# Kernel optimization log

Measured on AMD Instinct MI355X. Metric: run time of the kernel, lower is better.

## Reference

```python
import jax, jax.numpy as jnp
import numpy as np

N, E, IN, H, C, B, DD = 50000, 800000, 128, 4, 32, 64, 32
HC = H * C  # 128 = hidden_dim * num_heads


def setup_inputs() -> dict:
    key = jax.random.key(0)
    ks = jax.random.split(key, 28)
    r = lambda i, shape: jax.random.normal(ks[i], shape, jnp.float32) * 0.05
    return {
        "x": jax.random.normal(ks[0], (N, IN), jnp.float32),
        "domain": jax.random.normal(ks[1], (B, DD), jnp.float32),
        "Wl1": r(2, (HC, IN)), "bl1": r(3, (HC,)),
        "Wr1": r(4, (HC, IN)), "br1": r(5, (HC,)),
        "att1": r(6, (H, C)), "bias1": r(7, (HC,)),
        "Wl2": r(8, (HC, HC)), "bl2": r(9, (HC,)),
        "Wr2": r(10, (HC, HC)), "br2": r(11, (HC,)),
        "att2": r(12, (H, C)), "bias2": r(13, (HC,)),
        "Wres": r(14, (HC, IN)), "bres": r(15, (HC,)),
        "Wd": r(16, (64, DD)), "bd": r(17, (64,)),
        "Wg": r(18, (HC, HC)), "bg": r(19, (HC,)),
        "Wf1": r(20, (128, HC + 64)), "bf1": r(21, (128,)),
        "Wf2": r(22, (64, 128)), "bf2": r(23, (64,)),
        "Wf3": r(24, (1, 64)), "bf3": r(25, (1,)),
        "edge_index": jax.random.randint(ks[26], (2, E), 0, N),
        "batch": jnp.sort(jax.random.randint(ks[27], (N,), 0, B)),
    }


def gatv2_conv(x, src, dst, Wl, bl, Wr, br, att, bias):
    """PyG GATv2Conv, add_self_loops=False, concat heads, eval (no dropout)."""
    n = x.shape[0]
    xl = (x @ Wl.T + bl).reshape(n, H, C)  # source-side transform (lin_l)
    xr = (x @ Wr.T + br).reshape(n, H, C)  # target-side transform (lin_r)
    e = jax.nn.leaky_relu(xl[src] + xr[dst], 0.2)            # [E,H,C]
    s = jnp.einsum('ehc,hc->eh', e, att)                      # [E,H]
    smax = jax.ops.segment_max(s, dst, num_segments=n)        # per-dst max
    a = jnp.exp(s - smax[dst])
    denom = jax.ops.segment_sum(a, dst, num_segments=n)
    alpha = a / denom[dst]                                    # segment softmax
    out = jax.ops.segment_sum(alpha[:, :, None] * xl[src], dst, num_segments=n)
    return out.reshape(n, HC) + bias


def reference(x, domain, Wl1, bl1, Wr1, br1, att1, bias1,
              Wl2, bl2, Wr2, br2, att2, bias2,
              Wres, bres, Wd, bd, Wg, bg,
              Wf1, bf1, Wf2, bf2, Wf3, bf3,
              edge_index, batch):
    src, dst = edge_index[0], edge_index[1]
    res = x @ Wres.T + bres
    h = jax.nn.relu(gatv2_conv(x, src, dst, Wl1, bl1, Wr1, br1, att1, bias1)) + res
    h = jax.nn.relu(gatv2_conv(h, src, dst, Wl2, bl2, Wr2, br2, att2, bias2)) + h
    # global mean pool over graphs
    sums = jax.ops.segment_sum(h, batch, num_segments=B)
    counts = jax.ops.segment_sum(jnp.ones((h.shape[0],), h.dtype), batch, num_segments=B)
    pooled = sums / jnp.maximum(counts, 1.0)[:, None]
    g = jax.nn.relu(pooled @ Wg.T + bg)
    d = jax.nn.relu(domain @ Wd.T + bd)
    z = jnp.concatenate([g, d], axis=1)
    z = jax.nn.relu(z @ Wf1.T + bf1)
    z = jax.nn.relu(z @ Wf2.T + bf2)
    return (z @ Wf3.T + bf3).squeeze()
```

## Files before the change

### kernel.cpp

```cpp
#include <hip/hip_runtime.h>
#include <math.h>

#define NN 50000
#define NE 800000
#define FD 128
#define NB 64
#define NBUK 196
#define CHK 3125
#define NSC 1024
#define CHK2 782
#define CAP 6144
#define NBLK 782

typedef __attribute__((ext_vector_type(8))) short short8v;
typedef __attribute__((ext_vector_type(4))) float f32x4;
typedef _Float16 h2 __attribute__((ext_vector_type(2)));
typedef _Float16 h8 __attribute__((ext_vector_type(8)));

__device__ __forceinline__ unsigned short f2h(float f) {
  return __builtin_bit_cast(unsigned short, (_Float16)f);
}
__device__ __forceinline__ float h2f(unsigned short u) {
  return (float)__builtin_bit_cast(_Float16, u);
}

__device__ __forceinline__ size_t img_base(int n, int lane) {
  int lrow = n & 63, blk = n >> 6;
  int kh = lane >> 4, s7 = (lane >> 1) & 7, off4 = (lane & 1) * 4;
  return (size_t)blk * 8192 + kh * 4096 + lrow * 64 + 8 * (s7 ^ (lrow & 7)) + off4;
}

__global__ __launch_bounds__(256) void k_prep1(const float* __restrict__ W0,
    const float* __restrict__ W1, const float* __restrict__ W2,
    const float* __restrict__ W3, const float* __restrict__ W4,
    unsigned short* __restrict__ wh, unsigned short* __restrict__ wl,
    const int* __restrict__ dst, int* __restrict__ bcnt,
    const float* __restrict__ x, unsigned short* __restrict__ ximg) {
  __shared__ int bh[NBUK];
  int bx = blockIdx.x;
  if (bx < 256) {
    int t = threadIdx.x;
    for (int i = t; i < NBUK; i += 256) bh[i] = 0;
    __syncthreads();
    int e0 = bx * CHK, e1 = e0 + CHK;
    if (e1 > NE) e1 = NE;
    for (int e = e0 + t; e < e1; e += 256) atomicAdd(&bh[dst[e] >> 8], 1);
    __syncthreads();
    for (int i = t; i < NBUK; i += 256) if (bh[i]) atomicAdd(&bcnt[i], bh[i]);
  } else if (bx < 296) {
    int id = (bx - 256) * 256 + threadIdx.x;
    if (id >= 5 * 2048) return;
    int w = id >> 11, rem = id & 2047;
    int row = rem >> 4, slot = rem & 15;
    const float* Wp = (w == 0) ? W0 : (w == 1) ? W1 : (w == 2) ? W2 : (w == 3) ? W3 : W4;
    const float* sp = &Wp[row * 128 + slot * 8];
    int kh = slot >> 3, s7 = slot & 7;
    int d = ((w * 2 + kh) * 8192) + row * 64 + 8 * (s7 ^ (row & 7));
    short8v hi, lo;
    #pragma unroll
    for (int j = 0; j < 8; ++j) {
      float f = sp[j];
      _Float16 hv = (_Float16)f;
      _Float16 lv = (_Float16)(f - (float)hv);
      hi[j] = (short)__builtin_bit_cast(unsigned short, hv);
      lo[j] = (short)__builtin_bit_cast(unsigned short, lv);
    }
    *(short8v*)&wh[d] = hi;
    *(short8v*)&wl[d] = lo;
  } else {
    int id = (bx - 296) * 256 + threadIdx.x;
    int row = id >> 4, slot = id & 15;
    const float* sp = &x[(size_t)row * 128 + slot * 8];
    int blk = row >> 6, lrow = row & 63, kh = slot >> 3, s7 = slot & 7;
    size_t hoff = (size_t)blk * 8192 + kh * 4096 + lrow * 64 + 8 * (s7 ^ (lrow & 7));
    short8v hv;
    #pragma unroll
    for (int j = 0; j < 8; ++j)
      hv[j] = (short)f2h(sp[j]);
    *(short8v*)&ximg[hoff] = hv;
  }
}

__global__ __launch_bounds__(256) void k_bscan(const int* __restrict__ bcnt,
                                               int* __restrict__ bbase,
                                               int* __restrict__ bcur) {
  __shared__ int wsum[4];
  int t = threadIdx.x;
  int v = (t < NBUK) ? bcnt[t] : 0;
  int lane = t & 63, wv = t >> 6;
  int s = v;
  #pragma unroll
  for (int off = 1; off < 64; off <<= 1) {
    int y = __shfl_up(s, off, 64);
    if (lane >= off) s += y;
  }
  if (lane == 63) wsum[wv] = s;
  __syncthreads();
  if (t == 0) {
    int r = 0;
    #pragma unroll
    for (int i = 0; i < 4; ++i) { int x = wsum[i]; wsum[i] = r; r += x; }
  }
  __syncthreads();
  int excl = s - v + wsum[wv];
  if (t < NBUK) { bbase[t] = excl; bcur[t] = excl; }
  if (t == NBUK - 1) bbase[NBUK] = excl + v;
}

__global__ __launch_bounds__(256) void k_bscatter(const int* __restrict__ src,
    const int* __restrict__ dst, int* __restrict__ bcur, int* __restrict__ tmpv) {
  __shared__ int bh[NBUK];
  __shared__ int bb[NBUK];
  __shared__ int brun[NBUK];
  int t = threadIdx.x;
  int e0 = blockIdx.x * CHK2, e1 = e0 + CHK2;
  if (e1 > NE) e1 = NE;
  for (int i = t; i < NBUK; i += 256) { bh[i] = 0; brun[i] = 0; }
  __syncthreads();
  for (int e = e0 + t; e < e1; e += 256) atomicAdd(&bh[dst[e] >> 8], 1);
  __syncthreads();
  for (int i = t; i < NBUK; i += 256)
    bb[i] = bh[i] ? atomicAdd(&bcur[i], bh[i]) : 0;
  __syncthreads();
  for (int e = e0 + t; e < e1; e += 256) {
    int d = dst[e];
    int bk = d >> 8;
    int p = bb[bk] + atomicAdd(&brun[bk], 1);
    tmpv[p] = (src[e] << 8) | (d & 255);
  }
}

__device__ __forceinline__ void linm2_body(
    const unsigned short* __restrict__ aimg,
    const unsigned short* __restrict__ wh_img, const unsigned short* __restrict__ wl_img,
    int wimg, const float* __restrict__ bias,
    _Float16* __restrict__ out_h, int blk, char* smem) {
  unsigned short* s_a  = (unsigned short*)smem;
  unsigned short* s_wh = s_a + 4096;
  unsigned short* s_wl = s_wh + 8192;
  const int tid = threadIdx.x;
  const int lane = tid & 63;
  const int wv = tid >> 6;
  const int m0 = (wv >> 2) * 32;
  const int n0 = (wv & 3) * 32;
  const int rbase = blk * 64;
  const int g = lane >> 4, lr = lane & 15;

  f32x4 acc[2][2];
  #pragma unroll
  for (int mt = 0; mt < 2; ++mt)
    #pragma unroll
    for (int nt = 0; nt < 2; ++nt)
      acc[mt][nt] = (f32x4){0.f, 0.f, 0.f, 0.f};

  for (int kh = 0; kh < 2; ++kh) {
    if (kh) __syncthreads();
    {
      const short8v* asrc = (const short8v*)(aimg + (size_t)blk * 8192 + kh * 4096);
      ((short8v*)s_a)[tid] = asrc[tid];
    }
    {
      const short8v* whs = (const short8v*)(wh_img + (size_t)(wimg * 2 + kh) * 8192);
      const short8v* wls = (const short8v*)(wl_img + (size_t)(wimg * 2 + kh) * 8192);
      short8v* whd = (short8v*)s_wh;
      short8v* wld = (short8v*)s_wl;
      whd[tid] = whs[tid]; whd[512 + tid] = whs[512 + tid];
      wld[tid] = wls[tid]; wld[512 + tid] = wls[512 + tid];
    }
    __syncthreads();
    #pragma unroll
    for (int ks = 0; ks < 2; ++ks) {
      const int slot = ks * 4 + g;
      h8 a[2];
      #pragma unroll
      for (int mt = 0; mt < 2; ++mt) {
        int row = m0 + mt * 16 + lr;
        int idx = row * 64 + 8 * (slot ^ (row & 7));
        a[mt] = __builtin_bit_cast(h8, *(const short8v*)&s_a[idx]);
      }
      #pragma unroll
      for (int nt = 0; nt < 2; ++nt) {
        int row2 = n0 + nt * 16 + lr;
        int idx2 = row2 * 64 + 8 * (slot ^ (row2 & 7));
        h8 bh = __builtin_bit_cast(h8, *(const short8v*)&s_wh[idx2]);
        h8 bl = __builtin_bit_cast(h8, *(const short8v*)&s_wl[idx2]);
        #pragma unroll
        for (int mt = 0; mt < 2; ++mt) {
          acc[mt][nt] = __builtin_amdgcn_mfma_f32_16x16x32_f16(a[mt], bh, acc[mt][nt], 0, 0, 0);
          acc[mt][nt] = __builtin_amdgcn_mfma_f32_16x16x32_f16(a[mt], bl, acc[mt][nt], 0, 0, 0);
        }
      }
    }
  }
  #pragma unroll
  for (int nt = 0; nt < 2; ++nt) {
    float bv = bias[n0 + nt * 16 + lr];
    #pragma unroll
    for (int mt = 0; mt < 2; ++mt)
      #pragma unroll
      for (int i = 0; i < 4; ++i) {
        int r = rbase + m0 + mt * 16 + 4 * g + i;
        if (r < NN) {
          float vv = acc[mt][nt][i] + bv;
          out_h[(size_t)r * 128 + n0 + nt * 16 + lr] = (_Float16)vv;
        }
      }
  }
}

__global__ __launch_bounds__(512, 8) void k_csrlin(
    const int* __restrict__ tmpv, const int* __restrict__ bbase,
    int* __restrict__ offs, int* __restrict__ ssrc,
    const unsigned short* __restrict__ ximg,
    const unsigned short* __restrict__ wh_img, const unsigned short* __restrict__ wl_img,
    const float* __restrict__ bl1, const float* __restrict__ br1, const float* __restrict__ bres,
    _Float16* __restrict__ xl, _Float16* __restrict__ xr,
    _Float16* __restrict__ res) {
  __shared__ __align__(16) char smem[40960];
  int bx = blockIdx.x;
  if (bx < NBUK) {
    int* sdeg = (int*)smem;
    int* scur = sdeg + 256;
    int* wsum = scur + 256;
    int* lsrc = wsum + 16;
    int b = bx, t = threadIdx.x;
    int es = bbase[b], ee = bbase[b + 1];
    int cnt = ee - es;
    if (t < 256) sdeg[t] = 0;
    __syncthreads();
    for (int i = t; i < cnt; i += 512) atomicAdd(&sdeg[tmpv[es + i] & 255], 1);
    __syncthreads();
    int v = 0, s = 0;
    int lane = t & 63, wv = t >> 6;
    if (t < 256) {
      v = sdeg[t];
      s = v;
      #pragma unroll
      for (int off = 1; off < 64; off <<= 1) {
        int y = __shfl_up(s, off, 64);
        if (lane >= off) s += y;
      }
      if (lane == 63) wsum[wv] = s;
    }
    __syncthreads();
    if (t == 0) {
      int r = 0;
      #pragma unroll
      for (int i = 0; i < 4; ++i) { int x2 = wsum[i]; wsum[i] = r; r += x2; }
    }
    __syncthreads();
    if (t < 256) {
      int excl = s - v + wsum[wv];
      scur[t] = excl;
      int node = b * 256 + t;
      if (node < NN) offs[node] = es + excl;
    }
    if (b == 0 && t == 0) offs[NN] = NE;
    __syncthreads();
    if (cnt <= CAP) {
      for (int i = t; i < cnt; i += 512) {
        int pkt = tmpv[es + i];
        int p = atomicAdd(&scur[pkt & 255], 1);
        lsrc[p] = pkt >> 8;
      }
      __syncthreads();
      for (int i = t; i < cnt; i += 512) ssrc[es + i] = lsrc[i];
    } else {
      for (int i = t; i < cnt; i += 512) {
        int pkt = tmpv[es + i];
        int p = atomicAdd(&scur[pkt & 255], 1);
        ssrc[es + p] = pkt >> 8;
      }
    }
  } else {
    int bf = bx - NBUK;
    int w = bf / NBLK, blk = bf % NBLK;
    const float* bias = (w == 0) ? bl1 : (w == 1) ? br1 : bres;
    _Float16* oh = (w == 0) ? xl : (w == 1) ? xr : res;
    linm2_body(ximg, wh_img, wl_img, w, bias, oh, blk, smem);
  }
}

__global__ __launch_bounds__(512, 8) void k_lin2(
    const unsigned short* __restrict__ himg,
    const unsigned short* __restrict__ wh_img, const unsigned short* __restrict__ wl_img,
    const float* __restrict__ bl2, const float* __restrict__ br2,
    _Float16* __restrict__ xl, _Float16* __restrict__ xr) {
  __shared__ __align__(16) char smem[40960];
  int w = blockIdx.y;
  linm2_body(himg, wh_img, wl_img, 3 + w, (w == 0) ? bl2 : br2,
             (w == 0) ? xl : xr, blockIdx.x, smem);
}

__device__ __forceinline__ float4 gat_core(const _Float16* __restrict__ xl,
    const _Float16* __restrict__ xr, const int* __restrict__ offs,
    const int* __restrict__ ssrc, const float* __restrict__ att,
    const float* __restrict__ bias, int n, int lane) {
  float4 att4 = ((const float4*)att)[lane];
  h2 att01 = {(_Float16)att4.x, (_Float16)att4.y};
  h2 att23 = {(_Float16)att4.z, (_Float16)att4.w};
  uint2 xru = ((const uint2*)xr)[(size_t)n * 32 + lane];
  h2 xr01 = __builtin_bit_cast(h2, xru.x);
  h2 xr23 = __builtin_bit_cast(h2, xru.y);
  const h2 k02 = {(_Float16)0.2f, (_Float16)0.2f};
  int e0 = offs[n], e1 = offs[n + 1];
  float den = 0.f;
  float4 acc = make_float4(0.f, 0.f, 0.f, 0.f);
  int e = e0;
  for (; e + 3 < e1; e += 4) {
    uint2 u[4];
    #pragma unroll
    for (int j = 0; j < 4; ++j) {
      int s = ssrc[e + j];
      u[j] = ((const uint2*)xl)[(size_t)s * 32 + lane];
    }
    #pragma unroll
    for (int j = 0; j < 4; ++j) {
      h2 v01 = __builtin_bit_cast(h2, u[j].x);
      h2 v23 = __builtin_bit_cast(h2, u[j].y);
      h2 t01 = v01 + xr01;
      h2 t23 = v23 + xr23;
      h2 l01 = __builtin_elementwise_max(t01, t01 * k02);
      h2 l23 = __builtin_elementwise_max(t23, t23 * k02);
      float p = __builtin_amdgcn_fdot2(l01, att01, 0.f, false);
      p = __builtin_amdgcn_fdot2(l23, att23, p, false);
      p += __shfl_xor(p, 1, 64); p += __shfl_xor(p, 2, 64); p += __shfl_xor(p, 4, 64);
      float w = __expf(p);
      den += w;
      acc.x += w * (float)v01[0];
      acc.y += w * (float)v01[1];
      acc.z += w * (float)v23[0];
      acc.w += w * (float)v23[1];
    }
  }
  for (; e < e1; ++e) {
    int s = ssrc[e];
    uint2 uu = ((const uint2*)xl)[(size_t)s * 32 + lane];
    h2 v01 = __builtin_bit_cast(h2, uu.x);
    h2 v23 = __builtin_bit_cast(h2, uu.y);
    h2 t01 = v01 + xr01;
    h2 t23 = v23 + xr23;
    h2 l01 = __builtin_elementwise_max(t01, t01 * k02);
    h2 l23 = __builtin_elementwise_max(t23, t23 * k02);
    float p = __builtin_amdgcn_fdot2(l01, att01, 0.f, false);
    p = __builtin_amdgcn_fdot2(l23, att23, p, false);
    p += __shfl_xor(p, 1, 64); p += __shfl_xor(p, 2, 64); p += __shfl_xor(p, 4, 64);
    float w = __expf(p);
    den += w;
    acc.x += w * (float)v01[0];
    acc.y += w * (float)v01[1];
    acc.z += w * (float)v23[0];
    acc.w += w * (float)v23[1];
  }
  float inv = (den > 0.f) ? 1.f / den : 0.f;
  float4 b4 = ((const float4*)bias)[lane];
  float4 o;
  o.x = fmaxf(acc.x * inv + b4.x, 0.f);
  o.y = fmaxf(acc.y * inv + b4.y, 0.f);
  o.z = fmaxf(acc.z * inv + b4.z, 0.f);
  o.w = fmaxf(acc.w * inv + b4.w, 0.f);
  return o;
}

__global__ __launch_bounds__(256) void k_gat1(const _Float16* __restrict__ xl,
    const _Float16* __restrict__ xr, const int* __restrict__ offs,
    const int* __restrict__ ssrc, const float* __restrict__ att,
    const float* __restrict__ bias, const _Float16* __restrict__ resid,
    unsigned short* __restrict__ himg) {
  int grp = threadIdx.x >> 5;
  int lane = threadIdx.x & 31;
  int n = blockIdx.x * 8 + grp;
  float4 o = gat_core(xl, xr, offs, ssrc, att, bias, n, lane);
  uint2 ru = ((const uint2*)resid)[(size_t)n * 32 + lane];
  h2 r01 = __builtin_bit_cast(h2, ru.x);
  h2 r23 = __builtin_bit_cast(h2, ru.y);
  o.x += (float)r01[0]; o.y += (float)r01[1];
  o.z += (float)r23[0]; o.w += (float)r23[1];
  size_t base = img_base(n, lane);
  ushort4 hv;
  hv.x = f2h(o.x); hv.y = f2h(o.y); hv.z = f2h(o.z); hv.w = f2h(o.w);
  *(ushort4*)&himg[base] = hv;
}

__global__ __launch_bounds__(256) void k_gatpool(const _Float16* __restrict__ xl,
    const _Float16* __restrict__ xr, const int* __restrict__ offs,
    const int* __restrict__ ssrc, const float* __restrict__ att,
    const float* __restrict__ bias, const unsigned short* __restrict__ himg,
    const int* __restrict__ batch, float* __restrict__ pooled) {
  __shared__ float sm[8][128];
  __shared__ int sbat[8];
  int grp = threadIdx.x >> 5;
  int lane = threadIdx.x & 31;
  int n = blockIdx.x * 8 + grp;
  float4 o = gat_core(xl, xr, offs, ssrc, att, bias, n, lane);
  size_t base = img_base(n, lane);
  ushort4 rh = *(const ushort4*)&himg[base];
  o.x += h2f(rh.x); o.y += h2f(rh.y); o.z += h2f(rh.z); o.w += h2f(rh.w);
  *(float4*)&sm[grp][lane * 4] = o;
  if (threadIdx.x < 8) sbat[threadIdx.x] = batch[blockIdx.x * 8 + threadIdx.x];
  __syncthreads();
  int t = threadIdx.x;
  if (t < 128) {
    float run = sm[0][t];
    int cb = sbat[0];
    #pragma unroll
    for (int g2 = 1; g2 < 8; ++g2) {
      int bb = sbat[g2];
      if (bb != cb) { atomicAdd(&pooled[cb * FD + t], run); run = 0.f; cb = bb; }
      run += sm[g2][t];
    }
    atomicAdd(&pooled[cb * FD + t], run);
  }
}

__global__ __launch_bounds__(128) void k_mlp(const float* __restrict__ pooled,
    const int* __restrict__ batch, const float* __restrict__ domain,
    const float* __restrict__ Wg, const float* __restrict__ bg,
    const float* __restrict__ Wd, const float* __restrict__ bd,
    const float* __restrict__ Wf1, const float* __restrict__ bf1,
    const float* __restrict__ Wf2, const float* __restrict__ bf2,
    const float* __restrict__ Wf3, const float* __restrict__ bf3,
    float* __restrict__ out) {
  __shared__ float z[192];
  __shared__ float z1[128];
  __shared__ float z2[64];
  __shared__ float pm[128];
  __shared__ int cnt;
  int b = blockIdx.x, t = threadIdx.x;
  if (t == 0) {
    int lo = 0, hi = NN;
    while (lo < hi) { int mid = (lo + hi) >> 1; if (batch[mid] < b) lo = mid + 1; else hi = mid; }
    int lb = lo; lo = 0; hi = NN;
    while (lo < hi) { int mid = (lo + hi) >> 1; if (batch[mid] < b + 1) lo = mid + 1; else hi = mid; }
    cnt = lo - lb;
  }
  __syncthreads();
  float invc = 1.f / fmaxf((float)cnt, 1.f);
  pm[t] = pooled[b * FD + t] * invc;
  __syncthreads();
  {
    float a = bg[t];
    for (int k = 0; k < 128; ++k) a += pm[k] * Wg[t * 128 + k];
    z[t] = fmaxf(a, 0.f);
  }
  if (t < 64) {
    float a = bd[t];
    for (int k = 0; k < 32; ++k) a += domain[b * 32 + k] * Wd[t * 32 + k];
    z[128 + t] = fmaxf(a, 0.f);
  }
  __syncthreads();
  {
    float a = bf1[t];
    for (int k = 0; k < 192; ++k) a += z[k] * Wf1[t * 192 + k];
    z1[t] = fmaxf(a, 0.f);
  }
  __syncthreads();
  if (t < 64) {
    float a = bf2[t];
    for (int k = 0; k < 128; ++k) a += z1[k] * Wf2[t * 128 + k];
    z2[t] = fmaxf(a, 0.f);
  }
  __syncthreads();
  if (t < 64) {
    float v = z2[t] * Wf3[t];
    for (int off = 1; off < 64; off <<= 1) v += __shfl_xor(v, off, 64);
    if (t == 0) out[b] = v + bf3[0];
  }
}

extern "C" void kernel_launch(void* const* d_in, const int* in_sizes, int n_in,
                              void* d_out, int out_size, void* d_ws, size_t ws_size,
                              hipStream_t stream) {
  const float* x      = (const float*)d_in[0];
  const float* domain = (const float*)d_in[1];
  const float* Wl1 = (const float*)d_in[2];  const float* bl1 = (const float*)d_in[3];
  const float* Wr1 = (const float*)d_in[4];  const float* br1 = (const float*)d_in[5];
  const float* att1= (const float*)d_in[6];  const float* bias1=(const float*)d_in[7];
  const float* Wl2 = (const float*)d_in[8];  const float* bl2 = (const float*)d_in[9];
  const float* Wr2 = (const float*)d_in[10]; const float* br2 = (const float*)d_in[11];
  const float* att2= (const float*)d_in[12]; const float* bias2=(const float*)d_in[13];
  const float* Wres= (const float*)d_in[14]; const float* bres= (const float*)d_in[15];
  const float* Wd  = (const float*)d_in[16]; const float* bd  = (const float*)d_in[17];
  const float* Wg  = (const float*)d_in[18]; const float* bg  = (const float*)d_in[19];
  const float* Wf1 = (const float*)d_in[20]; const float* bf1 = (const float*)d_in[21];
  const float* Wf2 = (const float*)d_in[22]; const float* bf2 = (const float*)d_in[23];
  const float* Wf3 = (const float*)d_in[24]; const float* bf3 = (const float*)d_in[25];
  const int* ei    = (const int*)d_in[26];
  const int* batch = (const int*)d_in[27];
  const int* esrc = ei;
  const int* edst = ei + NE;
  float* outp = (float*)d_out;

  char* p = (char*)d_ws;
  auto carve = [&](size_t bytes) { char* r = p; p += (bytes + 255) & ~(size_t)255; return r; };
  int* bcnt     = (int*)carve((size_t)NBUK * 4);
  int* bbase    = (int*)carve((size_t)(NBUK + 1) * 4);
  int* bcur     = (int*)carve((size_t)NBUK * 4);
  int* tmpv     = (int*)carve((size_t)NE * 4);
  int* ssrc     = (int*)carve((size_t)NE * 4);
  int* offs     = (int*)carve((size_t)(NN + 1) * 4);
  unsigned short* wh = (unsigned short*)carve((size_t)5 * 2 * 8192 * 2);
  unsigned short* wl = (unsigned short*)carve((size_t)5 * 2 * 8192 * 2);
  unsigned short* ximg = (unsigned short*)carve((size_t)NBLK * 8192 * 2);
  _Float16* xl  = (_Float16*)carve((size_t)NN * FD * 2);
  _Float16* xr  = (_Float16*)carve((size_t)NN * FD * 2);
  _Float16* res = (_Float16*)carve((size_t)NN * FD * 2);
  float* pooled = (float*)carve((size_t)NB * FD * 4);
  unsigned short* himg = ximg;

  hipMemsetAsync(bcnt, 0, (size_t)NBUK * 4, stream);
  hipMemsetAsync(pooled, 0, (size_t)NB * FD * 4, stream);

  dim3 b256(256);
  hipLaunchKernelGGL(k_prep1, dim3(256 + 40 + 3125), b256, 0, stream,
                     Wl1, Wr1, Wres, Wl2, Wr2, wh, wl, edst, bcnt, x, ximg);
  hipLaunchKernelGGL(k_bscan, dim3(1), b256, 0, stream, bcnt, bbase, bcur);
  hipLaunchKernelGGL(k_bscatter, dim3(NSC), b256, 0, stream, esrc, edst, bcur, tmpv);
  hipLaunchKernelGGL(k_csrlin, dim3(NBUK + 3 * NBLK), dim3(512), 0, stream,
                     tmpv, bbase, offs, ssrc, ximg, wh, wl, bl1, br1, bres, xl, xr, res);
  hipLaunchKernelGGL(k_gat1, dim3(NN / 8), b256, 0, stream,
                     xl, xr, offs, ssrc, att1, bias1, res, himg);
  hipLaunchKernelGGL(k_lin2, dim3(NBLK, 2), dim3(512), 0, stream,
                     himg, wh, wl, bl2, br2, xl, xr);
  hipLaunchKernelGGL(k_gatpool, dim3(NN / 8), b256, 0, stream,
                     xl, xr, offs, ssrc, att2, bias2, himg, batch, pooled);
  hipLaunchKernelGGL(k_mlp, dim3(NB), dim3(128), 0, stream, pooled, batch, domain,
                     Wg, bg, Wd, bd, Wf1, bf1, Wf2, bf2, Wf3, bf3, outp);
}
```

Before: 186.6 us.

## Replace atomic bucket scatter with 2D histogram scan and unroll GAT gather by 8

The bucket-sort preprocessing now records a per-chunk histogram and column-scans it to get deterministic per-chunk offsets. This removes the second histogram pass and the global atomics in the scatter kernel, at the cost of one extra small kernel launch and fewer, larger scatter blocks (256 instead of 1024). It also adds an 8-way unrolled edge loop in the GAT core so more neighbor gathers are in flight, which raises register pressure.

```diff
diff --git a/kernel.cpp b/kernel.cpp
--- a/kernel.cpp
+++ b/kernel.cpp
@@ -6,9 +6,8 @@
 #define FD 128
 #define NB 64
 #define NBUK 196
+#define NCHK 256
 #define CHK 3125
-#define NSC 1024
-#define CHK2 782
 #define CAP 6144
 #define NBLK 782
 
@@ -34,11 +33,11 @@
     const float* __restrict__ W1, const float* __restrict__ W2,
     const float* __restrict__ W3, const float* __restrict__ W4,
     unsigned short* __restrict__ wh, unsigned short* __restrict__ wl,
-    const int* __restrict__ dst, int* __restrict__ bcnt,
+    const int* __restrict__ dst, int* __restrict__ hist2d,
     const float* __restrict__ x, unsigned short* __restrict__ ximg) {
   __shared__ int bh[NBUK];
   int bx = blockIdx.x;
-  if (bx < 256) {
+  if (bx < NCHK) {
     int t = threadIdx.x;
     for (int i = t; i < NBUK; i += 256) bh[i] = 0;
     __syncthreads();
@@ -46,9 +45,9 @@
     if (e1 > NE) e1 = NE;
     for (int e = e0 + t; e < e1; e += 256) atomicAdd(&bh[dst[e] >> 8], 1);
     __syncthreads();
-    for (int i = t; i < NBUK; i += 256) if (bh[i]) atomicAdd(&bcnt[i], bh[i]);
-  } else if (bx < 296) {
-    int id = (bx - 256) * 256 + threadIdx.x;
+    for (int i = t; i < NBUK; i += 256) hist2d[bx * NBUK + i] = bh[i];
+  } else if (bx < NCHK + 40) {
+    int id = (bx - NCHK) * 256 + threadIdx.x;
     if (id >= 5 * 2048) return;
     int w = id >> 11, rem = id & 2047;
     int row = rem >> 4, slot = rem & 15;
@@ -68,7 +67,7 @@
     *(short8v*)&wh[d] = hi;
     *(short8v*)&wl[d] = lo;
   } else {
-    int id = (bx - 296) * 256 + threadIdx.x;
+    int id = (bx - NCHK - 40) * 256 + threadIdx.x;
     int row = id >> 4, slot = id & 15;
     const float* sp = &x[(size_t)row * 128 + slot * 8];
     int blk = row >> 6, lrow = row & 63, kh = slot >> 3, s7 = slot & 7;
@@ -81,12 +80,11 @@
   }
 }
 
-__global__ __launch_bounds__(256) void k_bscan(const int* __restrict__ bcnt,
-                                               int* __restrict__ bbase,
-                                               int* __restrict__ bcur) {
-  __shared__ int wsum[4];
-  int t = threadIdx.x;
-  int v = (t < NBUK) ? bcnt[t] : 0;
+__global__ __launch_bounds__(256) void k_colscan(const int* __restrict__ hist2d,
+    int* __restrict__ coff, int* __restrict__ btot) {
+  __shared__ int ws[4];
+  int b = blockIdx.x, t = threadIdx.x;
+  int v = hist2d[t * NBUK + b];
   int lane = t & 63, wv = t >> 6;
   int s = v;
   #pragma unroll
@@ -94,34 +92,57 @@
     int y = __shfl_up(s, off, 64);
     if (lane >= off) s += y;
   }
-  if (lane == 63) wsum[wv] = s;
+  if (lane == 63) ws[wv] = s;
   __syncthreads();
   if (t == 0) {
     int r = 0;
     #pragma unroll
+    for (int i = 0; i < 4; ++i) { int x = ws[i]; ws[i] = r; r += x; }
+  }
+  __syncthreads();
+  int excl = s - v + ws[wv];
+  coff[b * 256 + t] = excl;
+  if (t == 255) btot[b] = excl + v;
+}
+
+__global__ __launch_bounds__(256) void k_bscan2(const int* __restrict__ btot,
+                                                int* __restrict__ bbase) {
+  __shared__ int wsum[4];
+  int t = threadIdx.x;
+  int v = (t < NBUK) ? btot[t] : 0;
+  int lane = t & 63, wv = t >> 6;
+  int s = v;
+  #pragma unroll
+  for (int off = 1; off < 64; off <<= 1) {
+    int y = __shfl_up(s, off, 64);
+    if (lane >= off) s += y;
+  }
+  if (lane == 63) wsum[wv] = s;
+  __syncthreads();
+  if (t == 0) {
+    int r = 0;
+    #pragma unroll
     for (int i = 0; i < 4; ++i) { int x = wsum[i]; wsum[i] = r; r += x; }
   }
   __syncthreads();
   int excl = s - v + wsum[wv];
-  if (t < NBUK) { bbase[t] = excl; bcur[t] = excl; }
+  if (t < NBUK) bbase[t] = excl;
   if (t == NBUK - 1) bbase[NBUK] = excl + v;
 }
 
 __global__ __launch_bounds__(256) void k_bscatter(const int* __restrict__ src,
-    const int* __restrict__ dst, int* __restrict__ bcur, int* __restrict__ tmpv) {
-  __shared__ int bh[NBUK];
+    const int* __restrict__ dst, const int* __restrict__ bbase,
+    const int* __restrict__ coff, int* __restrict__ tmpv) {
   __shared__ int bb[NBUK];
   __shared__ int brun[NBUK];
-  int t = threadIdx.x;
-  int e0 = blockIdx.x * CHK2, e1 = e0 + CHK2;
+  int c = blockIdx.x, t = threadIdx.x;
+  for (int i = t; i < NBUK; i += 256) {
+    bb[i] = bbase[i] + coff[i * 256 + c];
+    brun[i] = 0;
+  }
+  __syncthreads();
+  int e0 = c * CHK, e1 = e0 + CHK;
   if (e1 > NE) e1 = NE;
-  for (int i = t; i < NBUK; i += 256) { bh[i] = 0; brun[i] = 0; }
-  __syncthreads();
-  for (int e = e0 + t; e < e1; e += 256) atomicAdd(&bh[dst[e] >> 8], 1);
-  __syncthreads();
-  for (int i = t; i < NBUK; i += 256)
-    bb[i] = bh[i] ? atomicAdd(&bcur[i], bh[i]) : 0;
-  __syncthreads();
   for (int e = e0 + t; e < e1; e += 256) {
     int d = dst[e];
     int bk = d >> 8;
@@ -307,6 +328,32 @@
   float den = 0.f;
   float4 acc = make_float4(0.f, 0.f, 0.f, 0.f);
   int e = e0;
+  for (; e + 7 < e1; e += 8) {
+    uint2 u[8];
+    #pragma unroll
+    for (int j = 0; j < 8; ++j) {
+      int s = ssrc[e + j];
+      u[j] = ((const uint2*)xl)[(size_t)s * 32 + lane];
+    }
+    #pragma unroll
+    for (int j = 0; j < 8; ++j) {
+      h2 v01 = __builtin_bit_cast(h2, u[j].x);
+      h2 v23 = __builtin_bit_cast(h2, u[j].y);
+      h2 t01 = v01 + xr01;
+      h2 t23 = v23 + xr23;
+      h2 l01 = __builtin_elementwise_max(t01, t01 * k02);
+      h2 l23 = __builtin_elementwise_max(t23, t23 * k02);
+      float p = __builtin_amdgcn_fdot2(l01, att01, 0.f, false);
+      p = __builtin_amdgcn_fdot2(l23, att23, p, false);
+      p += __shfl_xor(p, 1, 64); p += __shfl_xor(p, 2, 64); p += __shfl_xor(p, 4, 64);
+      float w = __expf(p);
+      den += w;
+      acc.x += w * (float)v01[0];
+      acc.y += w * (float)v01[1];
+      acc.z += w * (float)v23[0];
+      acc.w += w * (float)v23[1];
+    }
+  }
   for (; e + 3 < e1; e += 4) {
     uint2 u[4];
     #pragma unroll
@@ -493,9 +540,10 @@
 
   char* p = (char*)d_ws;
   auto carve = [&](size_t bytes) { char* r = p; p += (bytes + 255) & ~(size_t)255; return r; };
-  int* bcnt     = (int*)carve((size_t)NBUK * 4);
+  int* hist2d   = (int*)carve((size_t)NCHK * NBUK * 4);
+  int* coff     = (int*)carve((size_t)NBUK * NCHK * 4);
+  int* btot     = (int*)carve((size_t)NBUK * 4);
   int* bbase    = (int*)carve((size_t)(NBUK + 1) * 4);
-  int* bcur     = (int*)carve((size_t)NBUK * 4);
   int* tmpv     = (int*)carve((size_t)NE * 4);
   int* ssrc     = (int*)carve((size_t)NE * 4);
   int* offs     = (int*)carve((size_t)(NN + 1) * 4);
@@ -508,14 +556,14 @@
   float* pooled = (float*)carve((size_t)NB * FD * 4);
   unsigned short* himg = ximg;
 
-  hipMemsetAsync(bcnt, 0, (size_t)NBUK * 4, stream);
   hipMemsetAsync(pooled, 0, (size_t)NB * FD * 4, stream);
 
   dim3 b256(256);
-  hipLaunchKernelGGL(k_prep1, dim3(256 + 40 + 3125), b256, 0, stream,
-                     Wl1, Wr1, Wres, Wl2, Wr2, wh, wl, edst, bcnt, x, ximg);
-  hipLaunchKernelGGL(k_bscan, dim3(1), b256, 0, stream, bcnt, bbase, bcur);
-  hipLaunchKernelGGL(k_bscatter, dim3(NSC), b256, 0, stream, esrc, edst, bcur, tmpv);
+  hipLaunchKernelGGL(k_prep1, dim3(NCHK + 40 + 3125), b256, 0, stream,
+                     Wl1, Wr1, Wres, Wl2, Wr2, wh, wl, edst, hist2d, x, ximg);
+  hipLaunchKernelGGL(k_colscan, dim3(NBUK), b256, 0, stream, hist2d, coff, btot);
+  hipLaunchKernelGGL(k_bscan2, dim3(1), b256, 0, stream, btot, bbase);
+  hipLaunchKernelGGL(k_bscatter, dim3(NCHK), b256, 0, stream, esrc, edst, bbase, coff, tmpv);
   hipLaunchKernelGGL(k_csrlin, dim3(NBUK + 3 * NBLK), dim3(512), 0, stream,
                      tmpv, bbase, offs, ssrc, ximg, wh, wl, bl1, br1, bres, xl, xr, res);
   hipLaunchKernelGGL(k_gat1, dim3(NN / 8), b256, 0, stream,
```

Result: no change. 184.1 us (-1.3%).
